# Performance work log

Measured on AMD Instinct MI355X. Metric: run time of the kernel, lower is better.

## Reference

```python
import jax, jax.numpy as jnp
import numpy as np

N_NODES = 50000
N_EDGES = 1600000
IN_SIZE = 128
NUM_HEADS = 4
OUT_SIZE = 32


def setup_inputs() -> dict:
    key = jax.random.key(0)
    k1, k2, k3, k4 = jax.random.split(key, 4)
    feat = jax.random.normal(k1, (N_NODES, IN_SIZE), dtype=jnp.float32)
    src = jax.random.randint(k2, (N_EDGES,), 0, N_NODES)
    dst = jnp.sort(jax.random.randint(k3, (N_EDGES,), 0, N_NODES))
    # fc weight of DGL DotGatConv: Linear(in_size, num_heads*out_size, bias=False)
    W = jax.random.normal(k4, (IN_SIZE, NUM_HEADS * OUT_SIZE), dtype=jnp.float32) * 0.05
    return {"feat": feat, "src": src, "dst": dst, "W": W}


def reference(feat, src, dst, W):
    N = feat.shape[0]
    H, D = NUM_HEADS, OUT_SIZE
    # project: [N, H, D]
    h = (feat @ W).reshape(N, H, D)
    h_src = h[src]            # [E, H, D] gather
    h_dst = h[dst]            # [E, H, D] gather
    # per-edge dot-product attention score, scaled by sqrt(out_size)
    e = jnp.sum(h_src * h_dst, axis=-1) / jnp.sqrt(jnp.asarray(D, h.dtype))  # [E, H]
    # edge softmax over incoming edges of each destination node
    m = jax.ops.segment_max(e, dst, num_segments=N)        # [N, H]
    ex = jnp.exp(e - m[dst])                               # [E, H]
    s = jax.ops.segment_sum(ex, dst, num_segments=N)       # [N, H]
    alpha = ex / s[dst]                                    # [E, H]
    # weighted aggregation of source features: sum_e alpha_e * h_src_e -> dst
    out = jax.ops.segment_sum(alpha[:, :, None] * h_src, dst, num_segments=N)  # [N, H, D]
    return out
```

## Files before the change

### kernel.cpp

```cpp
#include <hip/hip_runtime.h>
#include <math.h>

#define N_NODES 50000
#define N_EDGES 1600000
#define IN_SIZE 128
#define HD 128
#define NUM_HEADS 4
#define OUT_SIZE 32
#define STRIPS (N_NODES / 16)
#define STRIPS_PER_WAVE 3
#define PROJ_WAVES ((STRIPS + STRIPS_PER_WAVE - 1) / STRIPS_PER_WAVE)
#define PROJ_BLOCKS ((PROJ_WAVES + 3) / 4)
#define OFF_BLOCKS ((N_NODES + 1 + 255) / 256)

#define SCALE2 0.25503486f

typedef _Float16 half8 __attribute__((ext_vector_type(8)));
typedef _Float16 half2v __attribute__((ext_vector_type(2)));
typedef __attribute__((ext_vector_type(4))) float floatx4;

static __device__ __forceinline__ half2v pk_f16(float a, float b) {
#if __has_builtin(__builtin_amdgcn_cvt_pkrtz)
    auto r = __builtin_amdgcn_cvt_pkrtz(a, b);
    union { decltype(r) i; half2v o; } u;
    u.i = r;
    return u.o;
#else
    half2v r; r.x = (_Float16)a; r.y = (_Float16)b; return r;
#endif
}

static __device__ __forceinline__ float dot2(half2v a, half2v b, float c) {
#if __has_builtin(__builtin_amdgcn_fdot2)
    return __builtin_amdgcn_fdot2(a, b, c, false);
#else
    return fmaf((float)a.x, (float)b.x, fmaf((float)a.y, (float)b.y, c));
#endif
}

__global__ __launch_bounds__(256, 1) void k_pre(const float* __restrict__ feat,
                                                const float* __restrict__ W,
                                                const int* __restrict__ dst,
                                                _Float16* __restrict__ hb,
                                                int* __restrict__ off) {
    if (blockIdx.x >= PROJ_BLOCKS) {
        int i = (blockIdx.x - PROJ_BLOCKS) * 256 + threadIdx.x;
        if (i <= N_NODES) {
            int lo = 0, hi = N_EDGES;
            while (lo < hi) {
                int mid = (lo + hi) >> 1;
                if (dst[mid] < i) lo = mid + 1; else hi = mid;
            }
            off[i] = lo;
        }
        return;
    }

    int wid = blockIdx.x * 4 + (threadIdx.x >> 6);
    int lane = threadIdx.x & 63;
    int s0 = wid * STRIPS_PER_WAVE;
    if (s0 >= STRIPS) return;
    int quad = lane >> 4;
    int l15 = lane & 15;

    half8 Bf[8][4];
#pragma unroll
    for (int t = 0; t < 8; t++) {
#pragma unroll
        for (int kb = 0; kb < 4; kb++) {
            union { half8 v; half2v h[4]; } bu;
#pragma unroll
            for (int jj = 0; jj < 4; jj++) {
                int k0 = kb * 32 + quad * 8 + 2 * jj;
                float lo = W[(size_t)k0 * HD + t * 16 + l15];
                float hi = W[(size_t)(k0 + 1) * HD + t * 16 + l15];
                bu.h[jj] = pk_f16(lo, hi);
            }
            Bf[t][kb] = bu.v;
        }
    }

    for (int it = 0; it < STRIPS_PER_WAVE; it++) {
        int strip = s0 + it;
        if (strip >= STRIPS) break;
        int row = strip * 16 + l15;

        const float* ab = feat + (size_t)row * IN_SIZE + quad * 8;
        float4 a[8];
#pragma unroll
        for (int kb = 0; kb < 4; kb++) {
            a[2 * kb]     = *(const float4*)(ab + kb * 32);
            a[2 * kb + 1] = *(const float4*)(ab + kb * 32 + 4);
        }

        floatx4 acc[8];
#pragma unroll
        for (int t = 0; t < 8; t++) acc[t] = (floatx4)(0.f);

#pragma unroll
        for (int kb = 0; kb < 4; kb++) {
            float4 x = a[2 * kb], y = a[2 * kb + 1];
            union { half8 v; half2v h[4]; } af;
            af.h[0] = pk_f16(x.x, x.y);
            af.h[1] = pk_f16(x.z, x.w);
            af.h[2] = pk_f16(y.x, y.y);
            af.h[3] = pk_f16(y.z, y.w);
#pragma unroll
            for (int t = 0; t < 8; t++)
                acc[t] = __builtin_amdgcn_mfma_f32_16x16x32_f16(af.v, Bf[t][kb], acc[t], 0, 0, 0);
        }

#pragma unroll
        for (int t = 0; t < 8; t++) {
#pragma unroll
            for (int r = 0; r < 4; r++) {
                int R = strip * 16 + quad * 4 + r;
                hb[(size_t)R * HD + t * 16 + l15] = (_Float16)acc[t][r];
            }
        }
    }
}

__global__ __launch_bounds__(256) void k_edge(const _Float16* __restrict__ hb,
                                              const int* __restrict__ src,
                                              const int* __restrict__ off,
                                              float* __restrict__ out) {
    int n = (blockIdx.x * 256 + threadIdx.x) >> 6;
    int lane = threadIdx.x & 63;
    if (n >= N_NODES) return;
    int e0 = off[n], e1 = off[n + 1];

    int g = lane >> 4;
    int p = lane & 15;

    const uint4* h4 = (const uint4*)hb;
    union U { uint4 v; half2v h[4]; };

    U hdv; hdv.v = h4[(size_t)n * 16 + p];
    half2v hdc[4];
    half2v sc2 = pk_f16(SCALE2, SCALE2);
#pragma unroll
    for (int d = 0; d < 4; d++) hdc[d] = hdv.h[d] * sc2;

    float s = 0.f;
    half2v acc2[4];
#pragma unroll
    for (int d = 0; d < 4; d++) acc2[d] = (half2v)(_Float16)0.f;

    int iters = (e1 - e0 + 3) >> 2;
    int nloop = (iters + 1) >> 1;

    int ea = e0 + g;
    bool aa = (ea < e1);
    int sa = aa ? src[ea] : n;
    U va; va.v = h4[(size_t)sa * 16 + p];

    int eb = ea + 4;
    bool ab = (eb < e1);
    int sb = ab ? src[eb] : n;
    U vb; vb.v = h4[(size_t)sb * 16 + p];

    for (int it = 0; it < nloop; it++) {
        int ec = ea + 8;
        bool ac = (ec < e1);
        int scn = ac ? src[ec] : n;
        U vc; vc.v = h4[(size_t)scn * 16 + p];

        int ed = eb + 8;
        bool ad = (ed < e1);
        int sdn = ad ? src[ed] : n;
        U vd; vd.v = h4[(size_t)sdn * 16 + p];

        {
            float p0 = dot2(va.h[0], hdc[0], 0.f);
            float p1 = dot2(va.h[1], hdc[1], 0.f);
            p0 = dot2(va.h[2], hdc[2], p0);
            p1 = dot2(va.h[3], hdc[3], p1);
            float pd = p0 + p1;
            pd += __shfl_xor(pd, 1);
            pd += __shfl_xor(pd, 2);
            float w = aa ? __builtin_amdgcn_exp2f(pd) : 0.f;
            s += w;
            half2v wh = pk_f16(w, w);
#pragma unroll
            for (int d = 0; d < 4; d++) acc2[d] += va.h[d] * wh;
        }
        {
            float p0 = dot2(vb.h[0], hdc[0], 0.f);
            float p1 = dot2(vb.h[1], hdc[1], 0.f);
            p0 = dot2(vb.h[2], hdc[2], p0);
            p1 = dot2(vb.h[3], hdc[3], p1);
            float pd = p0 + p1;
            pd += __shfl_xor(pd, 1);
            pd += __shfl_xor(pd, 2);
            float w = ab ? __builtin_amdgcn_exp2f(pd) : 0.f;
            s += w;
            half2v wh = pk_f16(w, w);
#pragma unroll
            for (int d = 0; d < 4; d++) acc2[d] += vb.h[d] * wh;
        }

        va = vc; aa = ac; ea = ec;
        vb = vd; ab = ad; eb = ed;
    }

    union B { half2v h; int i; };
#pragma unroll
    for (int d = 16; d <= 32; d <<= 1) {
        s += __shfl_xor(s, d);
#pragma unroll
        for (int j = 0; j < 4; j++) {
            B b; b.h = acc2[j];
            b.i = __shfl_xor(b.i, d);
            acc2[j] += b.h;
        }
    }

    if (g == 0) {
        float inv = (s > 0.f) ? 1.f / s : 0.f;
        float4 o0, o1;
        o0.x = (float)acc2[0].x * inv; o0.y = (float)acc2[0].y * inv;
        o0.z = (float)acc2[1].x * inv; o0.w = (float)acc2[1].y * inv;
        o1.x = (float)acc2[2].x * inv; o1.y = (float)acc2[2].y * inv;
        o1.z = (float)acc2[3].x * inv; o1.w = (float)acc2[3].y * inv;
        float4* op = (float4*)(out + (size_t)n * HD + 8 * p);
        op[0] = o0;
        op[1] = o1;
    }
}

extern "C" void kernel_launch(void* const* d_in, const int* in_sizes, int n_in,
                              void* d_out, int out_size, void* d_ws, size_t ws_size,
                              hipStream_t stream) {
    const float* feat = (const float*)d_in[0];
    const int*   src  = (const int*)d_in[1];
    const int*   dst  = (const int*)d_in[2];
    const float* W    = (const float*)d_in[3];
    float* out = (float*)d_out;

    char* ws = (char*)d_ws;
    _Float16* hb = (_Float16*)ws;
    int* off = (int*)(ws + (size_t)N_NODES * HD * 2);

    k_pre<<<PROJ_BLOCKS + OFF_BLOCKS, 256, 0, stream>>>(feat, W, dst, hb, off);
    k_edge<<<(N_NODES + 3) / 4, 256, 0, stream>>>(hb, src, off, out);
}
```

Before: 146.7 us.

## Process eight edges per wave with eight lanes per row in edge kernel

Each lane now handles 16 halves (two uint4 loads) of a source row instead of 8, so a 64-lane wave covers 8 edges concurrently, with two edges in flight per lane-group per loop iteration. The per-head dot product needs one shuffle instead of two, the loop runs half as many iterations for high-degree nodes, and more gathers are in flight per wave. In exchange each lane holds more registers, the final cross-group reduction takes an extra shuffle round, and more lanes sit idle on nodes with few edges (average degree is about 32). Out-of-range edge indices are clamped to 0 before loading src.

```diff
diff --git a/kernel.cpp b/kernel.cpp
--- a/kernel.cpp
+++ b/kernel.cpp
@@ -130,74 +130,94 @@
     if (n >= N_NODES) return;
     int e0 = off[n], e1 = off[n + 1];
 
-    int g = lane >> 4;
-    int p = lane & 15;
+    int g = lane >> 3;
+    int p = lane & 7;
 
     const uint4* h4 = (const uint4*)hb;
-    union U { uint4 v; half2v h[4]; };
-
-    U hdv; hdv.v = h4[(size_t)n * 16 + p];
-    half2v hdc[4];
+    union U { uint4 v[2]; half2v h[8]; };
+
+    U hdv;
+    hdv.v[0] = h4[(size_t)n * 16 + 2 * p];
+    hdv.v[1] = h4[(size_t)n * 16 + 2 * p + 1];
+    half2v hdc[8];
     half2v sc2 = pk_f16(SCALE2, SCALE2);
 #pragma unroll
-    for (int d = 0; d < 4; d++) hdc[d] = hdv.h[d] * sc2;
+    for (int d = 0; d < 8; d++) hdc[d] = hdv.h[d] * sc2;
 
     float s = 0.f;
-    half2v acc2[4];
-#pragma unroll
-    for (int d = 0; d < 4; d++) acc2[d] = (half2v)(_Float16)0.f;
-
-    int iters = (e1 - e0 + 3) >> 2;
+    half2v acc2[8];
+#pragma unroll
+    for (int d = 0; d < 8; d++) acc2[d] = (half2v)(_Float16)0.f;
+
+    int iters = (e1 - e0 + 7) >> 3;
     int nloop = (iters + 1) >> 1;
 
     int ea = e0 + g;
     bool aa = (ea < e1);
-    int sa = aa ? src[ea] : n;
-    U va; va.v = h4[(size_t)sa * 16 + p];
-
-    int eb = ea + 4;
+    int eac = aa ? ea : 0;
+    int sa = aa ? src[eac] : n;
+    U va;
+    va.v[0] = h4[(size_t)sa * 16 + 2 * p];
+    va.v[1] = h4[(size_t)sa * 16 + 2 * p + 1];
+
+    int eb = ea + 8;
     bool ab = (eb < e1);
-    int sb = ab ? src[eb] : n;
-    U vb; vb.v = h4[(size_t)sb * 16 + p];
+    int ebc = ab ? eb : 0;
+    int sb = ab ? src[ebc] : n;
+    U vb;
+    vb.v[0] = h4[(size_t)sb * 16 + 2 * p];
+    vb.v[1] = h4[(size_t)sb * 16 + 2 * p + 1];
 
     for (int it = 0; it < nloop; it++) {
-        int ec = ea + 8;
+        int ec = ea + 16;
         bool ac = (ec < e1);
-        int scn = ac ? src[ec] : n;
-        U vc; vc.v = h4[(size_t)scn * 16 + p];
-
-        int ed = eb + 8;
+        int ecc = ac ? ec : 0;
+        int scn = ac ? src[ecc] : n;
+        U vc;
+        vc.v[0] = h4[(size_t)scn * 16 + 2 * p];
+        vc.v[1] = h4[(size_t)scn * 16 + 2 * p + 1];
+
+        int ed = eb + 16;
         bool ad = (ed < e1);
-        int sdn = ad ? src[ed] : n;
-        U vd; vd.v = h4[(size_t)sdn * 16 + p];
+        int edc = ad ? ed : 0;
+        int sdn = ad ? src[edc] : n;
+        U vd;
+        vd.v[0] = h4[(size_t)sdn * 16 + 2 * p];
+        vd.v[1] = h4[(size_t)sdn * 16 + 2 * p + 1];
 
         {
             float p0 = dot2(va.h[0], hdc[0], 0.f);
             float p1 = dot2(va.h[1], hdc[1], 0.f);
             p0 = dot2(va.h[2], hdc[2], p0);
             p1 = dot2(va.h[3], hdc[3], p1);
+            p0 = dot2(va.h[4], hdc[4], p0);
+            p1 = dot2(va.h[5], hdc[5], p1);
+            p0 = dot2(va.h[6], hdc[6], p0);
+            p1 = dot2(va.h[7], hdc[7], p1);
             float pd = p0 + p1;
             pd += __shfl_xor(pd, 1);
-            pd += __shfl_xor(pd, 2);
             float w = aa ? __builtin_amdgcn_exp2f(pd) : 0.f;
             s += w;
             half2v wh = pk_f16(w, w);
 #pragma unroll
-            for (int d = 0; d < 4; d++) acc2[d] += va.h[d] * wh;
+            for (int d = 0; d < 8; d++) acc2[d] += va.h[d] * wh;
         }
         {
             float p0 = dot2(vb.h[0], hdc[0], 0.f);
             float p1 = dot2(vb.h[1], hdc[1], 0.f);
             p0 = dot2(vb.h[2], hdc[2], p0);
             p1 = dot2(vb.h[3], hdc[3], p1);
+            p0 = dot2(vb.h[4], hdc[4], p0);
+            p1 = dot2(vb.h[5], hdc[5], p1);
+            p0 = dot2(vb.h[6], hdc[6], p0);
+            p1 = dot2(vb.h[7], hdc[7], p1);
             float pd = p0 + p1;
             pd += __shfl_xor(pd, 1);
-            pd += __shfl_xor(pd, 2);
             float w = ab ? __builtin_amdgcn_exp2f(pd) : 0.f;
             s += w;
             half2v wh = pk_f16(w, w);
 #pragma unroll
-            for (int d = 0; d < 4; d++) acc2[d] += vb.h[d] * wh;
+            for (int d = 0; d < 8; d++) acc2[d] += vb.h[d] * wh;
         }
 
         va = vc; aa = ac; ea = ec;
@@ -206,10 +226,10 @@
 
     union B { half2v h; int i; };
 #pragma unroll
-    for (int d = 16; d <= 32; d <<= 1) {
+    for (int d = 8; d <= 32; d <<= 1) {
         s += __shfl_xor(s, d);
 #pragma unroll
-        for (int j = 0; j < 4; j++) {
+        for (int j = 0; j < 8; j++) {
             B b; b.h = acc2[j];
             b.i = __shfl_xor(b.i, d);
             acc2[j] += b.h;
@@ -218,14 +238,16 @@
 
     if (g == 0) {
         float inv = (s > 0.f) ? 1.f / s : 0.f;
-        float4 o0, o1;
-        o0.x = (float)acc2[0].x * inv; o0.y = (float)acc2[0].y * inv;
-        o0.z = (float)acc2[1].x * inv; o0.w = (float)acc2[1].y * inv;
-        o1.x = (float)acc2[2].x * inv; o1.y = (float)acc2[2].y * inv;
-        o1.z = (float)acc2[3].x * inv; o1.w = (float)acc2[3].y * inv;
-        float4* op = (float4*)(out + (size_t)n * HD + 8 * p);
-        op[0] = o0;
-        op[1] = o1;
+        float4* op = (float4*)(out + (size_t)n * HD + 16 * p);
+#pragma unroll
+        for (int q = 0; q < 4; q++) {
+            float4 o;
+            o.x = (float)acc2[2 * q].x     * inv;
+            o.y = (float)acc2[2 * q].y     * inv;
+            o.z = (float)acc2[2 * q + 1].x * inv;
+            o.w = (float)acc2[2 * q + 1].y * inv;
+            op[q] = o;
+        }
     }
 }
 
```

After: 144.8 us. No clear change (-1.3%).

## Batch edge gathers per 64-edge chunk with shuffled src indices and 8-lane rows

Applied to the files above, without the earlier changes.

The edge kernel now loads 64 source indices at once with one coalesced load, broadcasts them with shuffles, and issues up to eight independent row gathers before any compute. Each lane now holds 32 bytes of a row (8 lanes per edge, 8 edges per pass) instead of 16 bytes (16 lanes per edge, 4 edges per pass). The final reduction becomes a transpose-style butterfly so every lane writes a float2 of the output. The aim is more memory-level parallelism and fewer dependent index loads, at the cost of more registers, which may lower occupancy.

```diff
diff --git a/kernel.cpp b/kernel.cpp
--- a/kernel.cpp
+++ b/kernel.cpp
@@ -36,6 +36,12 @@
 #else
     return fmaf((float)a.x, (float)b.x, fmaf((float)a.y, (float)b.y, c));
 #endif
+}
+
+static __device__ __forceinline__ half2v shflxor_h2(half2v x, int m) {
+    union { half2v h; int i; } u; u.h = x;
+    u.i = __shfl_xor(u.i, m);
+    return u.h;
 }
 
 __global__ __launch_bounds__(256, 1) void k_pre(const float* __restrict__ feat,
@@ -130,103 +136,105 @@
     if (n >= N_NODES) return;
     int e0 = off[n], e1 = off[n + 1];
 
-    int g = lane >> 4;
-    int p = lane & 15;
+    int g = lane >> 3;
+    int p = lane & 7;
 
     const uint4* h4 = (const uint4*)hb;
-    union U { uint4 v; half2v h[4]; };
-
-    U hdv; hdv.v = h4[(size_t)n * 16 + p];
-    half2v hdc[4];
+    union U { uint4 v[2]; half2v h[8]; };
+
+    const uint4* hrow = h4 + (size_t)n * 16;
+    U hdv;
+    hdv.v[0] = hrow[p];
+    hdv.v[1] = hrow[8 + p];
+    half2v hdc[8];
     half2v sc2 = pk_f16(SCALE2, SCALE2);
 #pragma unroll
-    for (int d = 0; d < 4; d++) hdc[d] = hdv.h[d] * sc2;
-
-    float s = 0.f;
-    half2v acc2[4];
-#pragma unroll
-    for (int d = 0; d < 4; d++) acc2[d] = (half2v)(_Float16)0.f;
-
-    int iters = (e1 - e0 + 3) >> 2;
-    int nloop = (iters + 1) >> 1;
-
-    int ea = e0 + g;
-    bool aa = (ea < e1);
-    int sa = aa ? src[ea] : n;
-    U va; va.v = h4[(size_t)sa * 16 + p];
-
-    int eb = ea + 4;
-    bool ab = (eb < e1);
-    int sb = ab ? src[eb] : n;
-    U vb; vb.v = h4[(size_t)sb * 16 + p];
-
-    for (int it = 0; it < nloop; it++) {
-        int ec = ea + 8;
-        bool ac = (ec < e1);
-        int scn = ac ? src[ec] : n;
-        U vc; vc.v = h4[(size_t)scn * 16 + p];
-
-        int ed = eb + 8;
-        bool ad = (ed < e1);
-        int sdn = ad ? src[ed] : n;
-        U vd; vd.v = h4[(size_t)sdn * 16 + p];
-
-        {
-            float p0 = dot2(va.h[0], hdc[0], 0.f);
-            float p1 = dot2(va.h[1], hdc[1], 0.f);
-            p0 = dot2(va.h[2], hdc[2], p0);
-            p1 = dot2(va.h[3], hdc[3], p1);
-            float pd = p0 + p1;
-            pd += __shfl_xor(pd, 1);
-            pd += __shfl_xor(pd, 2);
-            float w = aa ? __builtin_amdgcn_exp2f(pd) : 0.f;
-            s += w;
-            half2v wh = pk_f16(w, w);
-#pragma unroll
-            for (int d = 0; d < 4; d++) acc2[d] += va.h[d] * wh;
-        }
-        {
-            float p0 = dot2(vb.h[0], hdc[0], 0.f);
-            float p1 = dot2(vb.h[1], hdc[1], 0.f);
-            p0 = dot2(vb.h[2], hdc[2], p0);
-            p1 = dot2(vb.h[3], hdc[3], p1);
-            float pd = p0 + p1;
-            pd += __shfl_xor(pd, 1);
-            pd += __shfl_xor(pd, 2);
-            float w = ab ? __builtin_amdgcn_exp2f(pd) : 0.f;
-            s += w;
-            half2v wh = pk_f16(w, w);
-#pragma unroll
-            for (int d = 0; d < 4; d++) acc2[d] += vb.h[d] * wh;
-        }
-
-        va = vc; aa = ac; ea = ec;
-        vb = vd; ab = ad; eb = ed;
-    }
-
-    union B { half2v h; int i; };
-#pragma unroll
-    for (int d = 16; d <= 32; d <<= 1) {
-        s += __shfl_xor(s, d);
-#pragma unroll
-        for (int j = 0; j < 4; j++) {
-            B b; b.h = acc2[j];
-            b.i = __shfl_xor(b.i, d);
-            acc2[j] += b.h;
-        }
-    }
-
-    if (g == 0) {
-        float inv = (s > 0.f) ? 1.f / s : 0.f;
-        float4 o0, o1;
-        o0.x = (float)acc2[0].x * inv; o0.y = (float)acc2[0].y * inv;
-        o0.z = (float)acc2[1].x * inv; o0.w = (float)acc2[1].y * inv;
-        o1.x = (float)acc2[2].x * inv; o1.y = (float)acc2[2].y * inv;
-        o1.z = (float)acc2[3].x * inv; o1.w = (float)acc2[3].y * inv;
-        float4* op = (float4*)(out + (size_t)n * HD + 8 * p);
-        op[0] = o0;
-        op[1] = o1;
-    }
+    for (int d = 0; d < 8; d++) hdc[d] = hdv.h[d] * sc2;
+
+    float sA = 0.f, sB = 0.f;
+    half2v acc2[8];
+#pragma unroll
+    for (int d = 0; d < 8; d++) acc2[d] = (half2v)(_Float16)0.f;
+
+    for (int cb = e0; cb < e1; cb += 64) {
+        int m = e1 - cb;
+        if (m > 64) m = 64;
+        int li = (lane < m) ? lane : (m - 1);
+        int sv = src[cb + li];
+
+        U v[8];
+#pragma unroll
+        for (int k = 0; k < 8; k++) {
+            if (8 * k < m) {
+                int idx = __shfl(sv, 8 * k + g);
+                const uint4* rp = h4 + (size_t)idx * 16 + p;
+                v[k].v[0] = rp[0];
+                v[k].v[1] = rp[8];
+            }
+        }
+#pragma unroll
+        for (int k = 0; k < 8; k++) {
+            if (8 * k < m) {
+                bool valid = (8 * k + g) < m;
+                float a0 = dot2(v[k].h[0], hdc[0], 0.f);
+                float a1 = dot2(v[k].h[1], hdc[1], 0.f);
+                float b0 = dot2(v[k].h[4], hdc[4], 0.f);
+                float b1 = dot2(v[k].h[5], hdc[5], 0.f);
+                a0 = dot2(v[k].h[2], hdc[2], a0);
+                a1 = dot2(v[k].h[3], hdc[3], a1);
+                b0 = dot2(v[k].h[6], hdc[6], b0);
+                b1 = dot2(v[k].h[7], hdc[7], b1);
+                float pa = a0 + a1;
+                float pb = b0 + b1;
+                pa += __shfl_xor(pa, 1);
+                pb += __shfl_xor(pb, 1);
+                pa += __shfl_xor(pa, 2);
+                pb += __shfl_xor(pb, 2);
+                float wa = valid ? __builtin_amdgcn_exp2f(pa) : 0.f;
+                float wb = valid ? __builtin_amdgcn_exp2f(pb) : 0.f;
+                sA += wa;
+                sB += wb;
+                half2v wha = pk_f16(wa, wa);
+                half2v whb = pk_f16(wb, wb);
+#pragma unroll
+                for (int d = 0; d < 4; d++) acc2[d]     += v[k].h[d]     * wha;
+#pragma unroll
+                for (int d = 0; d < 4; d++) acc2[d + 4] += v[k].h[d + 4] * whb;
+            }
+        }
+    }
+
+    bool o1 = (g & 1) != 0, o2 = (g & 2) != 0, o4 = (g & 4) != 0;
+    half2v r1v[4];
+#pragma unroll
+    for (int j = 0; j < 4; j++) {
+        half2v kp = o1 ? acc2[j + 4] : acc2[j];
+        half2v sd = o1 ? acc2[j] : acc2[j + 4];
+        r1v[j] = kp + shflxor_h2(sd, 8);
+    }
+    half2v r2v[2];
+#pragma unroll
+    for (int j = 0; j < 2; j++) {
+        half2v kp = o2 ? r1v[j + 2] : r1v[j];
+        half2v sd = o2 ? r1v[j] : r1v[j + 2];
+        r2v[j] = kp + shflxor_h2(sd, 16);
+    }
+    half2v kp3 = o4 ? r2v[1] : r2v[0];
+    half2v sd3 = o4 ? r2v[0] : r2v[1];
+    half2v fin = kp3 + shflxor_h2(sd3, 32);
+
+    sA += __shfl_xor(sA, 8); sA += __shfl_xor(sA, 16); sA += __shfl_xor(sA, 32);
+    sB += __shfl_xor(sB, 8); sB += __shfl_xor(sB, 16); sB += __shfl_xor(sB, 32);
+    float invA = (sA > 0.f) ? 1.f / sA : 0.f;
+    float invB = (sB > 0.f) ? 1.f / sB : 0.f;
+    float inv = o1 ? invB : invA;
+
+    int wlo = ((g >> 1) & 1) * 2 + ((g >> 2) & 1);
+    int dim = (o1 ? 64 : 0) + 8 * p + 2 * wlo;
+    float2 o;
+    o.x = (float)fin.x * inv;
+    o.y = (float)fin.y * inv;
+    *(float2*)(out + (size_t)n * HD + dim) = o;
 }
 
 extern "C" void kernel_launch(void* const* d_in, const int* in_sizes, int n_in,
```

New measurement: 162.1 us. +10.5%, slower.
